# Kernel tuning notes

Measured on AMD Instinct MI355X. Metric: run time of the kernel, lower is better.

The kernel has to match this reference:

```python
import jax, jax.numpy as jnp
import numpy as np

ROWS, COLS, BATCH, NC, DEG = 256, 512, 512, 5, 16
N = (ROWS + COLS) * BATCH            # total nodes
E = ROWS * DEG * BATCH               # total edges
EPS = 1e-07

def _idx_sets():
    blk = np.arange(BATCH)[:, None] * (ROWS + COLS)
    idx_check = (blk + np.arange(ROWS)[None, :]).ravel()          # index_one
    idx_var = (blk + ROWS + np.arange(COLS)[None, :]).ravel()      # index_two
    return jnp.asarray(idx_check, jnp.int32), jnp.asarray(idx_var, jnp.int32)

IDX_CHECK, IDX_VAR = _idx_sets()

def setup_inputs() -> dict:
    key = jax.random.key(0)
    ks = jax.random.split(key, 18)
    rng = np.random.default_rng(0)
    # per-graph block offsets; row0 = check node ids, row1 = variable ids BEFORE the +ROWS shift
    offs = np.repeat(np.arange(BATCH) * (ROWS + COLS), ROWS * DEG)
    src = offs + rng.integers(0, ROWS, size=E)
    dst = offs + rng.integers(0, COLS, size=E)
    edge_index = jnp.asarray(np.stack([src, dst]), jnp.int32)
    x = jax.random.normal(ks[0], (N, 1), jnp.float32)

    def p(k, shape, fan):
        return (jax.random.uniform(k, shape, jnp.float32) * 2.0 - 1.0) / np.sqrt(fan)

    inp = {"x": x, "edge_index": edge_index}
    for li, base in ((1, 1), (2, 9)):
        inp[f"w1_{li}"] = p(ks[base + 0], (10, 2), 2)
        inp[f"b1_{li}"] = p(ks[base + 1], (10,), 2)
        inp[f"w2_{li}"] = p(ks[base + 2], (1, 10), 10)
        inp[f"b2_{li}"] = p(ks[base + 3], (1,), 10)
        inp[f"wih_{li}"] = p(ks[base + 4], (3, 1), 1)
        inp[f"whh_{li}"] = p(ks[base + 5], (3, 1), 1)
        inp[f"bih_{li}"] = p(ks[base + 6], (3,), 1)
        inp[f"bhh_{li}"] = p(ks[base + 7], (3,), 1)
    return inp

def _ggc(h, j_idx, i_idx, agg_idx, upd_idx, w1, b1, w2, b2, wih, whh, bih, bhh):
    # message: mlp(cat[x_j, x_i])
    feat = jnp.concatenate([h[j_idx], h[i_idx]], axis=1)          # [E,2]
    hid = jax.nn.relu(feat @ w1.T + b1)                            # [E,10]
    msg = hid @ w2.T + b2                                          # [E,1]
    m = jax.ops.segment_sum(msg, agg_idx, num_segments=N)          # scatter-add -> [N,1]
    # GRUCell(input=h[idx], hx=m[idx])   (note: original passes old state as INPUT, message as HIDDEN)
    xg = h[upd_idx]
    hx = m[upd_idx]
    gi = xg @ wih.T + bih                                          # [K,3]
    gh = hx @ whh.T + bhh                                          # [K,3]
    r = jax.nn.sigmoid(gi[:, 0:1] + gh[:, 0:1])
    z = jax.nn.sigmoid(gi[:, 1:2] + gh[:, 1:2])
    n = jnp.tanh(gi[:, 2:3] + r * gh[:, 2:3])
    hnew = (1.0 - z) * n + z * hx
    return h.at[upd_idx].set(hnew)

def reference(x, edge_index, w1_1, b1_1, w2_1, b2_1, wih_1, whh_1, bih_1, bhh_1,
              w1_2, b1_2, w2_2, b2_2, wih_2, whh_2, bih_2, bhh_2):
    src = edge_index[0]
    dst = edge_index[1] + ROWS          # shift variable ids into node index space
    h = x
    for _ in range(NC):
        # ggc1: source_to_target -> x_j=h[src], x_i=h[dst], aggregate at dst, update variable nodes
        h = _ggc(h, src, dst, dst, IDX_VAR, w1_1, b1_1, w2_1, b2_1, wih_1, whh_1, bih_1, bhh_1)
        # ggc2: target_to_source -> x_j=h[dst], x_i=h[src], aggregate at src, update check nodes
        h = _ggc(h, dst, src, src, IDX_CHECK, w1_2, b1_2, w2_2, b2_2, wih_2, whh_2, bih_2, bhh_2)
    return jnp.clip(jax.nn.sigmoid(-h), EPS, 1.0 - EPS)
```

## Files before the change

kernel.cpp:

```cpp
#include <hip/hip_runtime.h>

#define ROWS 256
#define COLS 512
#define BATCH 512
#define NC 5
#define DEG 16
#define EPG (ROWS * DEG)
#define NPG (ROWS + COLS)
#define NT 512
#define EPT (EPG / NT)
#define EPSF 1e-7f
#define SWZ(i) ((i) + ((i) >> 3))

typedef unsigned int u32;
typedef float v2f __attribute__((ext_vector_type(2)));

__device__ __forceinline__ float sigmoid_f(float a) {
    return 1.0f / (1.0f + __expf(-a));
}
__device__ __forceinline__ float tanh_f(float a) {
    return fmaf(2.0f, 1.0f / (1.0f + __expf(-2.0f * a)), -1.0f);
}

__global__ __launch_bounds__(NT, 4) void gnni_kernel(
    const float* __restrict__ x,
    const int*   __restrict__ eidx,
    const float* __restrict__ w1_1, const float* __restrict__ b1_1,
    const float* __restrict__ w2_1, const float* __restrict__ b2_1,
    const float* __restrict__ wih_1, const float* __restrict__ whh_1,
    const float* __restrict__ bih_1, const float* __restrict__ bhh_1,
    const float* __restrict__ w1_2, const float* __restrict__ b1_2,
    const float* __restrict__ w2_2, const float* __restrict__ b2_2,
    const float* __restrict__ wih_2, const float* __restrict__ whh_2,
    const float* __restrict__ bih_2, const float* __restrict__ bhh_2,
    float* __restrict__ out)
{
    __shared__ float msg[EPG + EPG / 8];
    __shared__ u32  cntd[COLS];
    __shared__ u32  cnts[ROWS];
    __shared__ unsigned short ofs_v[COLS + 1];
    __shared__ unsigned short ofs_c[ROWS + 1];
    __shared__ float hc[ROWS];
    __shared__ float hv[COLS];
    __shared__ u32  wsum[8];
    __shared__ u32  wsum2[4];

    const int tid  = threadIdx.x;
    const int lane = tid & 63;
    const int wid  = tid >> 6;
    const int b    = blockIdx.x;
    const int base = b * NPG;
    const long ebase = (long)b * EPG;

    const int4 sa = *(const int4*)(eidx + ebase + tid * 8);
    const int4 sb = *(const int4*)(eidx + ebase + tid * 8 + 4);
    const int4 da = *(const int4*)(eidx + (long)BATCH * EPG + ebase + tid * 8);
    const int4 db = *(const int4*)(eidx + (long)BATCH * EPG + ebase + tid * 8 + 4);
    const int sarr[EPT] = {sa.x, sa.y, sa.z, sa.w, sb.x, sb.y, sb.z, sb.w};
    const int darr[EPT] = {da.x, da.y, da.z, da.w, db.x, db.y, db.z, db.w};
    u32 ep[EPT];
    #pragma unroll
    for (int i = 0; i < EPT; ++i)
        ep[i] = (u32)(sarr[i] - base) | ((u32)(darr[i] - base) << 16);

    cntd[tid] = 0;
    if (tid < ROWS) cnts[tid] = 0;
    __syncthreads();
    #pragma unroll
    for (int i = 0; i < EPT; ++i) {
        atomicAdd(&cntd[ep[i] >> 16], 1u);
        atomicAdd(&cnts[ep[i] & 0xffffu], 1u);
    }
    __syncthreads();

    u32 myd = cntd[tid];
    u32 scv = myd;
    #pragma unroll
    for (int st = 1; st < 64; st <<= 1) {
        u32 t = __shfl_up(scv, st);
        if (lane >= st) scv += t;
    }
    if (lane == 63) wsum[wid] = scv;
    u32 mys = 0, scc = 0;
    if (tid < ROWS) {
        mys = cnts[tid];
        scc = mys;
        #pragma unroll
        for (int st = 1; st < 64; st <<= 1) {
            u32 t = __shfl_up(scc, st);
            if (lane >= st) scc += t;
        }
        if (lane == 63) wsum2[wid] = scc;
    }
    __syncthreads();
    if (tid < 8) {
        u32 v = wsum[tid];
        #pragma unroll
        for (int st = 1; st < 8; st <<= 1) {
            u32 t = __shfl_up(v, st);
            if (tid >= st) v += t;
        }
        wsum[tid] = v;
    } else if (tid < 12) {
        u32 v = wsum2[tid - 8];
        #pragma unroll
        for (int st = 1; st < 4; st <<= 1) {
            u32 t = __shfl_up(v, st);
            if (tid - 8 >= st) v += t;
        }
        wsum2[tid - 8] = v;
    }
    __syncthreads();
    {
        u32 inc = scv + (wid ? wsum[wid - 1] : 0u);
        ofs_v[tid + 1] = (unsigned short)inc;
        if (tid == 0) ofs_v[0] = 0;
        cntd[tid] = inc - myd;
    }
    if (tid < ROWS) {
        u32 inc = scc + (wid ? wsum2[wid - 1] : 0u);
        ofs_c[tid + 1] = (unsigned short)inc;
        if (tid == 0) ofs_c[0] = 0;
        cnts[tid] = inc - mys;
        hc[tid] = x[base + tid];
    }
    float hvreg = x[base + ROWS + tid];
    hv[tid] = hvreg;
    __syncthreads();

    u32 pos1[EPT], pos2[EPT];
    #pragma unroll
    for (int i = 0; i < EPT; ++i) {
        pos1[i] = atomicAdd(&cntd[ep[i] >> 16], 1u);
        pos2[i] = atomicAdd(&cnts[ep[i] & 0xffffu], 1u);
    }

    v2f A1[5], C1[5], B1[5], W1[5], A2[5], C2[5], B2[5], W2[5];
    #pragma unroll
    for (int j = 0; j < 5; ++j) {
        A1[j] = (v2f){w1_1[4*j],     w1_1[4*j + 2]};
        C1[j] = (v2f){w1_1[4*j + 1], w1_1[4*j + 3]};
        B1[j] = (v2f){b1_1[2*j],     b1_1[2*j + 1]};
        W1[j] = (v2f){w2_1[2*j],     w2_1[2*j + 1]};
        A2[j] = (v2f){w1_2[4*j],     w1_2[4*j + 2]};
        C2[j] = (v2f){w1_2[4*j + 1], w1_2[4*j + 3]};
        B2[j] = (v2f){b1_2[2*j],     b1_2[2*j + 1]};
        W2[j] = (v2f){w2_2[2*j],     w2_2[2*j + 1]};
    }
    const float b2_1s = b2_1[0], b2_2s = b2_2[0];
    const v2f zero2 = (v2f){0.0f, 0.0f};

    for (int it = 0; it < NC; ++it) {
        #pragma unroll
        for (int i = 0; i < EPT; ++i) {
            const u32 p = ep[i];
            const float xj = hc[p & 0xffffu];
            const float xi = hv[p >> 16];
            const v2f xj2 = (v2f){xj, xj}, xi2 = (v2f){xi, xi};
            v2f acc = (v2f){b2_1s, 0.0f};
            #pragma unroll
            for (int j = 0; j < 5; ++j) {
                v2f t = __builtin_elementwise_fma(C1[j], xi2, B1[j]);
                t = __builtin_elementwise_fma(A1[j], xj2, t);
                t = __builtin_elementwise_max(t, zero2);
                acc = __builtin_elementwise_fma(W1[j], t, acc);
            }
            msg[SWZ(pos1[i])] = acc.x + acc.y;
        }
        __syncthreads();

        {
            const int beg = ofs_v[tid], end = ofs_v[tid + 1];
            float hx = 0.0f;
            for (int e = beg; e < end; ++e) hx += msg[SWZ(e)];
            const float xg = hvreg;
            float gi0 = fmaf(wih_1[0], xg, bih_1[0]);
            float gi1 = fmaf(wih_1[1], xg, bih_1[1]);
            float gi2 = fmaf(wih_1[2], xg, bih_1[2]);
            float gh0 = fmaf(whh_1[0], hx, bhh_1[0]);
            float gh1 = fmaf(whh_1[1], hx, bhh_1[1]);
            float gh2 = fmaf(whh_1[2], hx, bhh_1[2]);
            float r = sigmoid_f(gi0 + gh0);
            float z = sigmoid_f(gi1 + gh1);
            float n = tanh_f(fmaf(r, gh2, gi2));
            hvreg = fmaf(1.0f - z, n, z * hx);
            hv[tid] = hvreg;
        }
        __syncthreads();

        #pragma unroll
        for (int i = 0; i < EPT; ++i) {
            const u32 p = ep[i];
            const float xi = hc[p & 0xffffu];
            const float xj = hv[p >> 16];
            const v2f xj2 = (v2f){xj, xj}, xi2 = (v2f){xi, xi};
            v2f acc = (v2f){b2_2s, 0.0f};
            #pragma unroll
            for (int j = 0; j < 5; ++j) {
                v2f t = __builtin_elementwise_fma(C2[j], xi2, B2[j]);
                t = __builtin_elementwise_fma(A2[j], xj2, t);
                t = __builtin_elementwise_max(t, zero2);
                acc = __builtin_elementwise_fma(W2[j], t, acc);
            }
            msg[SWZ(pos2[i])] = acc.x + acc.y;
        }
        __syncthreads();

        {
            const int c    = tid >> 1;
            const int half = tid & 1;
            const int beg = ofs_c[c], end = ofs_c[c + 1];
            const int h0  = (end - beg + 1) >> 1;
            const int lo  = half ? (beg + h0) : beg;
            const int hi  = half ? end : (beg + h0);
            float part = 0.0f;
            for (int e = lo; e < hi; ++e) part += msg[SWZ(e)];
            part += __shfl_xor(part, 1);
            if (half == 0) {
                const float hx = part;
                const float xg = hc[c];
                float gi0 = fmaf(wih_2[0], xg, bih_2[0]);
                float gi1 = fmaf(wih_2[1], xg, bih_2[1]);
                float gi2 = fmaf(wih_2[2], xg, bih_2[2]);
                float gh0 = fmaf(whh_2[0], hx, bhh_2[0]);
                float gh1 = fmaf(whh_2[1], hx, bhh_2[1]);
                float gh2 = fmaf(whh_2[2], hx, bhh_2[2]);
                float r = sigmoid_f(gi0 + gh0);
                float z = sigmoid_f(gi1 + gh1);
                float n = tanh_f(fmaf(r, gh2, gi2));
                hc[c] = fmaf(1.0f - z, n, z * hx);
            }
        }
        __syncthreads();
    }

    {
        float sgm = 1.0f / (1.0f + __expf(hvreg));
        out[base + ROWS + tid] = fminf(fmaxf(sgm, EPSF), 1.0f - EPSF);
    }
    if (tid < ROWS) {
        float sgm = 1.0f / (1.0f + __expf(hc[tid]));
        out[base + tid] = fminf(fmaxf(sgm, EPSF), 1.0f - EPSF);
    }
}

extern "C" void kernel_launch(void* const* d_in, const int* in_sizes, int n_in,
                              void* d_out, int out_size, void* d_ws, size_t ws_size,
                              hipStream_t stream) {
    const float* x    = (const float*)d_in[0];
    const int*   eidx = (const int*)d_in[1];
    gnni_kernel<<<BATCH, NT, 0, stream>>>(
        x, eidx,
        (const float*)d_in[2],  (const float*)d_in[3],
        (const float*)d_in[4],  (const float*)d_in[5],
        (const float*)d_in[6],  (const float*)d_in[7],
        (const float*)d_in[8],  (const float*)d_in[9],
        (const float*)d_in[10], (const float*)d_in[11],
        (const float*)d_in[12], (const float*)d_in[13],
        (const float*)d_in[14], (const float*)d_in[15],
        (const float*)d_in[16], (const float*)d_in[17],
        (float*)d_out);
}
```

Baseline: 43.39 us.

## Pre-sort edges by destination so message writes become contiguous vector stores

```diff
diff --git a/kernel.cpp b/kernel.cpp
--- a/kernel.cpp
+++ b/kernel.cpp
@@ -10,7 +10,8 @@
 #define NT 512
 #define EPT (EPG / NT)
 #define EPSF 1e-7f
-#define SWZ(i) ((i) + ((i) >> 3))
+#define SWZ(p) (((p) >> 3) * 10 + ((p) & 7))
+#define MSGW (EPG / 8 * 10)
 
 typedef unsigned int u32;
 typedef float v2f __attribute__((ext_vector_type(2)));
@@ -35,7 +36,9 @@
     const float* __restrict__ bih_2, const float* __restrict__ bhh_2,
     float* __restrict__ out)
 {
-    __shared__ float msg[EPG + EPG / 8];
+    __shared__ u32  e1[EPG];
+    __shared__ u32  e2[EPG];
+    __shared__ float msg[MSGW];
     __shared__ u32  cntd[COLS];
     __shared__ u32  cnts[ROWS];
     __shared__ unsigned short ofs_v[COLS + 1];
@@ -128,11 +131,29 @@
     hv[tid] = hvreg;
     __syncthreads();
 
-    u32 pos1[EPT], pos2[EPT];
     #pragma unroll
     for (int i = 0; i < EPT; ++i) {
-        pos1[i] = atomicAdd(&cntd[ep[i] >> 16], 1u);
-        pos2[i] = atomicAdd(&cnts[ep[i] & 0xffffu], 1u);
+        u32 p = ep[i];
+        u32 pos = atomicAdd(&cntd[p >> 16], 1u);
+        e1[pos] = p;
+        u32 pos2 = atomicAdd(&cnts[p & 0xffffu], 1u);
+        e2[pos2] = p;
+    }
+    __syncthreads();
+
+    u32 d1[EPT], s1[EPT], d2[EPT], s2[EPT];
+    {
+        const uint4 q0 = *(const uint4*)&e1[tid * 8];
+        const uint4 q1 = *(const uint4*)&e1[tid * 8 + 4];
+        const uint4 r0 = *(const uint4*)&e2[tid * 8];
+        const uint4 r1 = *(const uint4*)&e2[tid * 8 + 4];
+        const u32 eq1[EPT] = {q0.x,q0.y,q0.z,q0.w,q1.x,q1.y,q1.z,q1.w};
+        const u32 eq2[EPT] = {r0.x,r0.y,r0.z,r0.w,r1.x,r1.y,r1.z,r1.w};
+        #pragma unroll
+        for (int i = 0; i < EPT; ++i) {
+            d1[i] = eq1[i] >> 16;  s1[i] = eq1[i] & 0xffffu;
+            d2[i] = eq2[i] >> 16;  s2[i] = eq2[i] & 0xffffu;
+        }
     }
 
     v2f A1[5], C1[5], B1[5], W1[5], A2[5], C2[5], B2[5], W2[5];
@@ -149,23 +170,30 @@
     }
     const float b2_1s = b2_1[0], b2_2s = b2_2[0];
     const v2f zero2 = (v2f){0.0f, 0.0f};
+    float2* const mbase = (float2*)&msg[tid * 10];
 
     for (int it = 0; it < NC; ++it) {
-        #pragma unroll
-        for (int i = 0; i < EPT; ++i) {
-            const u32 p = ep[i];
-            const float xj = hc[p & 0xffffu];
-            const float xi = hv[p >> 16];
-            const v2f xj2 = (v2f){xj, xj}, xi2 = (v2f){xi, xi};
-            v2f acc = (v2f){b2_1s, 0.0f};
+        {
+            float m[EPT];
             #pragma unroll
-            for (int j = 0; j < 5; ++j) {
-                v2f t = __builtin_elementwise_fma(C1[j], xi2, B1[j]);
-                t = __builtin_elementwise_fma(A1[j], xj2, t);
-                t = __builtin_elementwise_max(t, zero2);
-                acc = __builtin_elementwise_fma(W1[j], t, acc);
+            for (int i = 0; i < EPT; ++i) {
+                const float xj = hc[s1[i]];
+                const float xi = hv[d1[i]];
+                const v2f xj2 = (v2f){xj, xj}, xi2 = (v2f){xi, xi};
+                v2f acc = (v2f){b2_1s, 0.0f};
+                #pragma unroll
+                for (int j = 0; j < 5; ++j) {
+                    v2f t = __builtin_elementwise_fma(C1[j], xi2, B1[j]);
+                    t = __builtin_elementwise_fma(A1[j], xj2, t);
+                    t = __builtin_elementwise_max(t, zero2);
+                    acc = __builtin_elementwise_fma(W1[j], t, acc);
+                }
+                m[i] = acc.x + acc.y;
             }
-            msg[SWZ(pos1[i])] = acc.x + acc.y;
+            mbase[0] = (float2){m[0], m[1]};
+            mbase[1] = (float2){m[2], m[3]};
+            mbase[2] = (float2){m[4], m[5]};
+            mbase[3] = (float2){m[6], m[7]};
         }
         __syncthreads();
 
@@ -188,21 +216,27 @@
         }
         __syncthreads();
 
-        #pragma unroll
-        for (int i = 0; i < EPT; ++i) {
-            const u32 p = ep[i];
-            const float xi = hc[p & 0xffffu];
-            const float xj = hv[p >> 16];
-            const v2f xj2 = (v2f){xj, xj}, xi2 = (v2f){xi, xi};
-            v2f acc = (v2f){b2_2s, 0.0f};
+        {
+            float m[EPT];
             #pragma unroll
-            for (int j = 0; j < 5; ++j) {
-                v2f t = __builtin_elementwise_fma(C2[j], xi2, B2[j]);
-                t = __builtin_elementwise_fma(A2[j], xj2, t);
-                t = __builtin_elementwise_max(t, zero2);
-                acc = __builtin_elementwise_fma(W2[j], t, acc);
+            for (int i = 0; i < EPT; ++i) {
+                const float xj = hv[d2[i]];
+                const float xi = hc[s2[i]];
+                const v2f xj2 = (v2f){xj, xj}, xi2 = (v2f){xi, xi};
+                v2f acc = (v2f){b2_2s, 0.0f};
+                #pragma unroll
+                for (int j = 0; j < 5; ++j) {
+                    v2f t = __builtin_elementwise_fma(C2[j], xi2, B2[j]);
+                    t = __builtin_elementwise_fma(A2[j], xj2, t);
+                    t = __builtin_elementwise_max(t, zero2);
+                    acc = __builtin_elementwise_fma(W2[j], t, acc);
+                }
+                m[i] = acc.x + acc.y;
             }
-            msg[SWZ(pos2[i])] = acc.x + acc.y;
+            mbase[0] = (float2){m[0], m[1]};
+            mbase[1] = (float2){m[2], m[3]};
+            mbase[2] = (float2){m[4], m[5]};
+            mbase[3] = (float2){m[6], m[7]};
         }
         __syncthreads();
 
```

After: 45.09 us. +3.9%, slower.
